# Optimization experiments

Hardware: AMD Instinct MI355X
Metric: run time of the kernel (lower is better)

## Reference

```python
import jax, jax.numpy as jnp
import numpy as np

NEG_SLOPE = 0.2
EPS = 1e-16
N_NODES = 50000
N_EDGES = 800000
D_IN = 128
D_E = 64
HEADS = 4
D_OUT = 32


def setup_inputs() -> dict:
    key = jax.random.key(0)
    k1, k2, k3, k4, k5, k6 = jax.random.split(key, 6)
    H = jax.random.normal(k1, (N_NODES, D_IN), dtype=jnp.float32)
    edge_index = jax.random.randint(k2, (2, N_EDGES), 0, N_NODES, dtype=jnp.int64)
    E = jax.random.normal(k3, (N_EDGES, D_E), dtype=jnp.float32)
    # torch nn.Linear weights: [out_features, in_features]
    W = jax.random.normal(k4, (HEADS * D_OUT, D_IN), dtype=jnp.float32) * (1.0 / np.sqrt(D_IN))
    W_e = jax.random.normal(k5, (HEADS * D_OUT, D_E), dtype=jnp.float32) * (1.0 / np.sqrt(D_E))
    att = jax.random.normal(k6, (1, HEADS, D_OUT), dtype=jnp.float32) * 0.1
    return {"H": H, "edge_index": edge_index, "E": E, "W": W, "W_e": W_e, "att": att}


def reference(H, edge_index, E, W, W_e, att):
    n_nodes = H.shape[0]
    # node transform: [N, heads, d_out]
    HT = (H @ W.T).reshape(n_nodes, HEADS, D_OUT)
    src, dst = edge_index[0], edge_index[1]
    # edge transform: [E, heads, d_out]
    ET = (E @ W_e.T).reshape(-1, HEADS, D_OUT)
    alpha_in = HT[src] + HT[dst] + ET              # [E, heads, d_out]
    alpha_in = jax.nn.leaky_relu(alpha_in, NEG_SLOPE)
    alpha = jnp.sum(alpha_in * att, axis=-1)        # [E, heads]
    # segment softmax over incoming edges of each dst node
    a_max = jax.ops.segment_max(alpha, dst, num_segments=n_nodes)   # [N, heads]
    alpha = jnp.exp(alpha - a_max[dst])
    a_sum = jax.ops.segment_sum(alpha, dst, num_segments=n_nodes)   # [N, heads]
    alpha = alpha / (a_sum[dst] + EPS)
    # weighted aggregation of source features
    messages = HT[src] * alpha[:, :, None]          # [E, heads, d_out]
    H_out = jax.ops.segment_sum(messages, dst, num_segments=n_nodes)  # [N, heads, d_out]
    return H_out.reshape(n_nodes, HEADS * D_OUT)    # concat=True
```

## Files before the change

kernel.cpp:

```cpp
#include <hip/hip_runtime.h>

#define N_NODES 50000
#define N_EDGES 800000
#define D_IN    128
#define D_E     64
#define NH      4
#define F_TOT   128
#define NEG_SLOPE 0.2f

typedef __attribute__((ext_vector_type(8))) short short8;
typedef __attribute__((ext_vector_type(4))) float f32x4;

__device__ __forceinline__ short f2bf(float x) {
    unsigned u = __float_as_uint(x);
    u += 0x7FFFu + ((u >> 16) & 1u);
    return (short)(u >> 16);
}

__global__ __launch_bounds__(256) void k_node_transform(
    const float* __restrict__ H, const float* __restrict__ W,
    float* __restrict__ HT)
{
    __shared__ float wt[D_IN * F_TOT];
    const int tid = threadIdx.x;
    for (int i = tid; i < D_IN * F_TOT; i += 256) {
        const int f = i & 127, k = i >> 7;
        wt[k * F_TOT + f] = W[f * D_IN + k];
    }
    __syncthreads();

    const int l = tid & 63;
    const int w = tid >> 6;
    const int gwave  = blockIdx.x * 4 + w;
    const int nwaves = gridDim.x * 4;
    const int ngroups = N_NODES / 8;

    for (int grp = gwave; grp < ngroups; grp += nwaves) {
        const int g = grp * 8;
        float ax[8], ay[8];
#pragma unroll
        for (int j = 0; j < 8; ++j) { ax[j] = 0.f; ay[j] = 0.f; }

        for (int k4 = 0; k4 < D_IN / 4; ++k4) {
            float hv[8][4];
#pragma unroll
            for (int j = 0; j < 8; ++j)
                *(float4*)hv[j] = *(const float4*)&H[(size_t)(g + j) * D_IN + k4 * 4];
#pragma unroll
            for (int kk = 0; kk < 4; ++kk) {
                const float2 wk = *(const float2*)&wt[(k4 * 4 + kk) * F_TOT + 2 * l];
#pragma unroll
                for (int j = 0; j < 8; ++j) {
                    ax[j] = fmaf(wk.x, hv[j][kk], ax[j]);
                    ay[j] = fmaf(wk.y, hv[j][kk], ay[j]);
                }
            }
        }
#pragma unroll
        for (int j = 0; j < 8; ++j) {
            float2 r; r.x = ax[j]; r.y = ay[j];
            *(float2*)&HT[(size_t)(g + j) * F_TOT + 2 * l] = r;
        }
    }
}

__global__ __launch_bounds__(256) void k_hist(
    const int* __restrict__ EI, int* __restrict__ deg)
{
    const int e = blockIdx.x * 256 + threadIdx.x;
    if (e < N_EDGES) atomicAdd(&deg[EI[N_EDGES + e]], 1);
}

__global__ __launch_bounds__(1024) void k_scan(
    const int* __restrict__ deg, int* __restrict__ row_start,
    int* __restrict__ cursor)
{
    __shared__ int wsum[16];
    __shared__ int carry;
    const int tid = threadIdx.x;
    const int l = tid & 63;
    const int wv = tid >> 6;
    if (tid == 0) carry = 0;

    for (int base = 0; base < N_NODES; base += 1024) {
        __syncthreads();
        const int cb = carry;
        const int i = base + tid;
        const int v = (i < N_NODES) ? deg[i] : 0;
        int x = v;
#pragma unroll
        for (int off = 1; off < 64; off <<= 1) {
            int t = __shfl_up(x, off, 64);
            if (l >= off) x += t;
        }
        if (l == 63) wsum[wv] = x;
        __syncthreads();
        int wave_off = 0;
        for (int k = 0; k < wv; ++k) wave_off += wsum[k];
        int tot = 0;
#pragma unroll
        for (int k = 0; k < 16; ++k) tot += wsum[k];
        const int excl = cb + wave_off + (x - v);
        if (i < N_NODES) { row_start[i] = excl; cursor[i] = excl; }
        __syncthreads();
        if (tid == 0) carry = cb + tot;
    }
    __syncthreads();
    if (tid == 0) row_start[N_NODES] = carry;
}

__global__ __launch_bounds__(256, 3) void k_logits(
    const float* __restrict__ E, const int* __restrict__ EI,
    const float* __restrict__ We, const float* __restrict__ att,
    const float* __restrict__ HT,
    float* __restrict__ wperm, int* __restrict__ srcperm,
    int* __restrict__ cursor)
{
    const int tid = threadIdx.x;
    const int l   = tid & 63;
    const int wv  = tid >> 6;
    const int r16 = l & 15;
    const int g4  = l >> 4;

    short8 bf[8][2];
#pragma unroll
    for (int ft = 0; ft < 8; ++ft) {
#pragma unroll
        for (int kc = 0; kc < 2; ++kc) {
            const float* wp = &We[(size_t)(ft * 16 + r16) * D_E + kc * 32 + g4 * 8];
            const float4 lo = *(const float4*)wp;
            const float4 hi = *(const float4*)(wp + 4);
            short8 b;
            b[0] = f2bf(lo.x); b[1] = f2bf(lo.y); b[2] = f2bf(lo.z); b[3] = f2bf(lo.w);
            b[4] = f2bf(hi.x); b[5] = f2bf(hi.y); b[6] = f2bf(hi.z); b[7] = f2bf(hi.w);
            bf[ft][kc] = b;
        }
    }
    float attv[8];
#pragma unroll
    for (int ft = 0; ft < 8; ++ft) attv[ft] = att[ft * 16 + r16];

    const int gwave  = blockIdx.x * 4 + wv;
    const int nwaves = gridDim.x * 4;
    const int ntiles = N_EDGES / 16;

    for (int t = gwave; t < ntiles; t += nwaves) {
        const int e0 = t * 16;
        short8 af[2];
#pragma unroll
        for (int kc = 0; kc < 2; ++kc) {
            const float* ep = &E[(size_t)(e0 + r16) * D_E + kc * 32 + g4 * 8];
            const float4 lo = *(const float4*)ep;
            const float4 hi = *(const float4*)(ep + 4);
            short8 a;
            a[0] = f2bf(lo.x); a[1] = f2bf(lo.y); a[2] = f2bf(lo.z); a[3] = f2bf(lo.w);
            a[4] = f2bf(hi.x); a[5] = f2bf(hi.y); a[6] = f2bf(hi.z); a[7] = f2bf(hi.w);
            af[kc] = a;
        }
        f32x4 acc[8];
#pragma unroll
        for (int ft = 0; ft < 8; ++ft) {
            f32x4 z = {0.f, 0.f, 0.f, 0.f};
            z = __builtin_amdgcn_mfma_f32_16x16x32_bf16(af[0], bf[ft][0], z, 0, 0, 0);
            acc[ft] = __builtin_amdgcn_mfma_f32_16x16x32_bf16(af[1], bf[ft][1], z, 0, 0, 0);
        }
        int sr_[4], dr_[4];
#pragma unroll
        for (int r = 0; r < 4; ++r) {
            sr_[r] = EI[e0 + g4 * 4 + r];
            dr_[r] = EI[N_EDGES + e0 + g4 * 4 + r];
        }
#pragma unroll
        for (int r = 0; r < 4; ++r) {
            const int sr = sr_[r], dr = dr_[r];
            float ph[4] = {0.f, 0.f, 0.f, 0.f};
#pragma unroll
            for (int ft = 0; ft < 8; ++ft) {
                const float hs = HT[(size_t)sr * F_TOT + ft * 16 + r16];
                const float hd = HT[(size_t)dr * F_TOT + ft * 16 + r16];
                float v = hs + hd + acc[ft][r];
                v = v > 0.f ? v : NEG_SLOPE * v;
                ph[ft >> 1] = fmaf(v, attv[ft], ph[ft >> 1]);
            }
#pragma unroll
            for (int m = 1; m < 16; m <<= 1) {
#pragma unroll
                for (int hh = 0; hh < 4; ++hh)
                    ph[hh] += __shfl_xor(ph[hh], m, 64);
            }
            const float w0 = __expf(ph[0]), w1 = __expf(ph[1]);
            const float w2 = __expf(ph[2]), w3 = __expf(ph[3]);
            int pos = 0;
            if (r16 == 0) pos = atomicAdd(&cursor[dr], 1);
            pos = __shfl(pos, l & 48, 64);
            if (r16 < 4) {
                const float wv_ = r16 == 0 ? w0 : r16 == 1 ? w1 : r16 == 2 ? w2 : w3;
                wperm[4 * pos + r16] = wv_;
            }
            if (r16 == 4) srcperm[pos] = sr;
        }
    }
}

__global__ __launch_bounds__(256, 8) void k_aggregate(
    const float* __restrict__ HT, const float* __restrict__ wperm,
    const int* __restrict__ srcperm, const int* __restrict__ row_start,
    float* __restrict__ out)
{
    const int tid = threadIdx.x;
    const int l = tid & 63;
    const int wv = tid >> 6;
    const int n = blockIdx.x * 4 + wv;
    if (n >= N_NODES) return;
    const int h = l >> 4;
    const int beg = row_start[n];
    const int end = row_start[n + 1];

    float ax = 0.f, ay = 0.f, sw = 0.f;
    for (int base = beg; base < end; base += 16) {
        const int   svl = (l < 16 && base + l < end) ? srcperm[base + l] : 0;
        const float wvl = (4 * base + l < 4 * end) ? wperm[4 * base + l] : 0.f;
#pragma unroll
        for (int j = 0; j < 16; ++j) {
            const int   s = __shfl(svl, j, 64);
            const float w = __shfl(wvl, 4 * j + h, 64);
            const float2 hs = *(const float2*)&HT[(size_t)s * F_TOT + 2 * l];
            ax = fmaf(w, hs.x, ax);
            ay = fmaf(w, hs.y, ay);
            sw += w;
        }
    }
    const float inv = 1.f / (sw + 1e-16f);
    float2 r; r.x = ax * inv; r.y = ay * inv;
    *(float2*)&out[(size_t)n * F_TOT + 2 * l] = r;
}

extern "C" void kernel_launch(void* const* d_in, const int* in_sizes, int n_in,
                              void* d_out, int out_size, void* d_ws, size_t ws_size,
                              hipStream_t stream)
{
    const float* H   = (const float*)d_in[0];
    const int*   EI  = (const int*)d_in[1];
    const float* E   = (const float*)d_in[2];
    const float* W   = (const float*)d_in[3];
    const float* We  = (const float*)d_in[4];
    const float* att = (const float*)d_in[5];
    float* out = (float*)d_out;

    float* HT        = (float*)d_ws;
    float* wperm     = HT + (size_t)N_NODES * F_TOT;
    int*   srcperm   = (int*)(wperm + (size_t)N_EDGES * NH);
    int*   deg       = srcperm + N_EDGES;
    int*   row_start = deg + N_NODES;
    int*   cursor    = row_start + N_NODES + 1;

    hipMemsetAsync(deg, 0, N_NODES * sizeof(int), stream);

    k_hist<<<(N_EDGES + 255) / 256, 256, 0, stream>>>(EI, deg);
    k_scan<<<1, 1024, 0, stream>>>(deg, row_start, cursor);
    k_node_transform<<<512, 256, 0, stream>>>(H, W, HT);
    k_logits<<<1024, 256, 0, stream>>>(E, EI, We, att, HT,
                                       wperm, srcperm, cursor);
    k_aggregate<<<(N_NODES + 3) / 4, 256, 0, stream>>>(HT, wperm, srcperm,
                                                       row_start, out);
}
```

Baseline: 691.3 us.

## Transpose MFMA operands in edge-logit kernel so each lane owns one edge

Swaps the MFMA operand order so the output tile has features along lanes and edges along columns. Each lane then gathers contiguous float4 chunks of HT for a single edge instead of scalar loads across four edges. This cuts the head reduction to two shuffles and lets 16 lanes do one atomic and one vector store each. The bf16 weights and attention vectors move from per-lane registers into shared memory, filled once per block. The grid is doubled to use the lower register pressure.

Measured after the change: 669.0 us. 3.2% less time.

```diff
diff --git a/kernel.cpp b/kernel.cpp
--- a/kernel.cpp
+++ b/kernel.cpp
@@ -116,29 +116,35 @@
     float* __restrict__ wperm, int* __restrict__ srcperm,
     int* __restrict__ cursor)
 {
+    __shared__ short8 s_bf[8][2][64];
+    __shared__ f32x4  s_att[8][4];
+
     const int tid = threadIdx.x;
     const int l   = tid & 63;
     const int wv  = tid >> 6;
     const int r16 = l & 15;
     const int g4  = l >> 4;
 
-    short8 bf[8][2];
-#pragma unroll
-    for (int ft = 0; ft < 8; ++ft) {
-#pragma unroll
-        for (int kc = 0; kc < 2; ++kc) {
-            const float* wp = &We[(size_t)(ft * 16 + r16) * D_E + kc * 32 + g4 * 8];
-            const float4 lo = *(const float4*)wp;
-            const float4 hi = *(const float4*)(wp + 4);
-            short8 b;
-            b[0] = f2bf(lo.x); b[1] = f2bf(lo.y); b[2] = f2bf(lo.z); b[3] = f2bf(lo.w);
-            b[4] = f2bf(hi.x); b[5] = f2bf(hi.y); b[6] = f2bf(hi.z); b[7] = f2bf(hi.w);
-            bf[ft][kc] = b;
-        }
-    }
-    float attv[8];
-#pragma unroll
-    for (int ft = 0; ft < 8; ++ft) attv[ft] = att[ft * 16 + r16];
+    if (wv == 0) {
+#pragma unroll
+        for (int ft = 0; ft < 8; ++ft) {
+#pragma unroll
+            for (int kc = 0; kc < 2; ++kc) {
+                const float* wp = &We[(size_t)(ft * 16 + r16) * D_E + kc * 32 + g4 * 8];
+                const f32x4 lo = *(const f32x4*)wp;
+                const f32x4 hi = *(const f32x4*)(wp + 4);
+                short8 b;
+                b[0] = f2bf(lo[0]); b[1] = f2bf(lo[1]); b[2] = f2bf(lo[2]); b[3] = f2bf(lo[3]);
+                b[4] = f2bf(hi[0]); b[5] = f2bf(hi[1]); b[6] = f2bf(hi[2]); b[7] = f2bf(hi[3]);
+                s_bf[ft][kc][l] = b;
+            }
+        }
+        if (l < 32) {
+            const int ft = l >> 2, g = l & 3;
+            s_att[ft][g] = *(const f32x4*)&att[ft * 16 + g * 4];
+        }
+    }
+    __syncthreads();
 
     const int gwave  = blockIdx.x * 4 + wv;
     const int nwaves = gridDim.x * 4;
@@ -146,58 +152,60 @@
 
     for (int t = gwave; t < ntiles; t += nwaves) {
         const int e0 = t * 16;
+        const int e  = e0 + r16;
+        const int sr = EI[e];
+        const int dr = EI[N_EDGES + e];
+
+        int pos = 0;
+        if (l < 16) pos = atomicAdd(&cursor[dr], 1);
+
+        const float* hsp = &HT[(size_t)sr * F_TOT + g4 * 4];
+        const float* hdp = &HT[(size_t)dr * F_TOT + g4 * 4];
+        f32x4 hs4[8], hd4[8];
+#pragma unroll
+        for (int ft = 0; ft < 8; ++ft) {
+            hs4[ft] = *(const f32x4*)(hsp + ft * 16);
+            hd4[ft] = *(const f32x4*)(hdp + ft * 16);
+        }
+
         short8 af[2];
 #pragma unroll
         for (int kc = 0; kc < 2; ++kc) {
-            const float* ep = &E[(size_t)(e0 + r16) * D_E + kc * 32 + g4 * 8];
-            const float4 lo = *(const float4*)ep;
-            const float4 hi = *(const float4*)(ep + 4);
+            const float* ep = &E[(size_t)e * D_E + kc * 32 + g4 * 8];
+            const f32x4 lo = *(const f32x4*)ep;
+            const f32x4 hi = *(const f32x4*)(ep + 4);
             short8 a;
-            a[0] = f2bf(lo.x); a[1] = f2bf(lo.y); a[2] = f2bf(lo.z); a[3] = f2bf(lo.w);
-            a[4] = f2bf(hi.x); a[5] = f2bf(hi.y); a[6] = f2bf(hi.z); a[7] = f2bf(hi.w);
+            a[0] = f2bf(lo[0]); a[1] = f2bf(lo[1]); a[2] = f2bf(lo[2]); a[3] = f2bf(lo[3]);
+            a[4] = f2bf(hi[0]); a[5] = f2bf(hi[1]); a[6] = f2bf(hi[2]); a[7] = f2bf(hi[3]);
             af[kc] = a;
         }
-        f32x4 acc[8];
+
+        float ph[4] = {0.f, 0.f, 0.f, 0.f};
 #pragma unroll
         for (int ft = 0; ft < 8; ++ft) {
             f32x4 z = {0.f, 0.f, 0.f, 0.f};
-            z = __builtin_amdgcn_mfma_f32_16x16x32_bf16(af[0], bf[ft][0], z, 0, 0, 0);
-            acc[ft] = __builtin_amdgcn_mfma_f32_16x16x32_bf16(af[1], bf[ft][1], z, 0, 0, 0);
-        }
-        int sr_[4], dr_[4];
-#pragma unroll
-        for (int r = 0; r < 4; ++r) {
-            sr_[r] = EI[e0 + g4 * 4 + r];
-            dr_[r] = EI[N_EDGES + e0 + g4 * 4 + r];
-        }
-#pragma unroll
-        for (int r = 0; r < 4; ++r) {
-            const int sr = sr_[r], dr = dr_[r];
-            float ph[4] = {0.f, 0.f, 0.f, 0.f};
-#pragma unroll
-            for (int ft = 0; ft < 8; ++ft) {
-                const float hs = HT[(size_t)sr * F_TOT + ft * 16 + r16];
-                const float hd = HT[(size_t)dr * F_TOT + ft * 16 + r16];
-                float v = hs + hd + acc[ft][r];
+            z = __builtin_amdgcn_mfma_f32_16x16x32_bf16(s_bf[ft][0][l], af[0], z, 0, 0, 0);
+            const f32x4 acc =
+                __builtin_amdgcn_mfma_f32_16x16x32_bf16(s_bf[ft][1][l], af[1], z, 0, 0, 0);
+            const f32x4 at = s_att[ft][g4];
+#pragma unroll
+            for (int r = 0; r < 4; ++r) {
+                float v = hs4[ft][r] + hd4[ft][r] + acc[r];
                 v = v > 0.f ? v : NEG_SLOPE * v;
-                ph[ft >> 1] = fmaf(v, attv[ft], ph[ft >> 1]);
+                ph[ft >> 1] = fmaf(v, at[r], ph[ft >> 1]);
             }
-#pragma unroll
-            for (int m = 1; m < 16; m <<= 1) {
-#pragma unroll
-                for (int hh = 0; hh < 4; ++hh)
-                    ph[hh] += __shfl_xor(ph[hh], m, 64);
-            }
-            const float w0 = __expf(ph[0]), w1 = __expf(ph[1]);
-            const float w2 = __expf(ph[2]), w3 = __expf(ph[3]);
-            int pos = 0;
-            if (r16 == 0) pos = atomicAdd(&cursor[dr], 1);
-            pos = __shfl(pos, l & 48, 64);
-            if (r16 < 4) {
-                const float wv_ = r16 == 0 ? w0 : r16 == 1 ? w1 : r16 == 2 ? w2 : w3;
-                wperm[4 * pos + r16] = wv_;
-            }
-            if (r16 == 4) srcperm[pos] = sr;
+        }
+#pragma unroll
+        for (int h = 0; h < 4; ++h) {
+            ph[h] += __shfl_xor(ph[h], 16, 64);
+            ph[h] += __shfl_xor(ph[h], 32, 64);
+        }
+        if (l < 16) {
+            f32x4 w;
+            w[0] = __expf(ph[0]); w[1] = __expf(ph[1]);
+            w[2] = __expf(ph[2]); w[3] = __expf(ph[3]);
+            *(f32x4*)&wperm[(size_t)4 * pos] = w;
+            srcperm[pos] = sr;
         }
     }
 }
@@ -259,7 +267,7 @@
     k_hist<<<(N_EDGES + 255) / 256, 256, 0, stream>>>(EI, deg);
     k_scan<<<1, 1024, 0, stream>>>(deg, row_start, cursor);
     k_node_transform<<<512, 256, 0, stream>>>(H, W, HT);
-    k_logits<<<1024, 256, 0, stream>>>(E, EI, We, att, HT,
+    k_logits<<<2048, 256, 0, stream>>>(E, EI, We, att, HT,
                                        wperm, srcperm, cursor);
     k_aggregate<<<(N_NODES + 3) / 4, 256, 0, stream>>>(HT, wperm, srcperm,
                                                        row_start, out);
```
